# Performance work log

Measured on AMD Instinct MI355X. Metric: run time of the kernel, lower is better.

## Reference

```python
import jax, jax.numpy as jnp
import numpy as np

# Routing structure from the torch module
GT0 = [[0,1,0,0,1,0],[0,1,0,0,0,1],[0,0,1,0,1,0],[0,0,1,0,0,1],[0,0,0,1,1,0],[0,0,0,1,0,1]]
NCLS = 6
K = 1  # top-k

def _expert_pairs():
    # For class i, expert index m = 1+(j-1)*5+(k-1) maps to atom1[j-1] -> atom2[k-1].
    pairs = []
    for i in range(NCLS):
        p = [(j - 1, k - 1) for j in range(1, 6) for k in range(1, 6)
             if j != k and GT0[i][j] == 1 and GT0[i][k] == 1]
        pairs.append(p)
    return pairs

PAIRS = _expert_pairs()  # each class has exactly 2 (atom1, atom2) pairs

B, P, D, H = 64, 256, 768, 3072

def setup_inputs() -> dict:
    key = jax.random.key(0)
    ks = jax.random.split(key, 8)
    s = 0.02
    x = jax.random.normal(ks[0], (B, NCLS + P, D), dtype=jnp.float32)
    mids = jax.random.randint(ks[1], (B,), 0, 6)
    moe0_W1 = jax.random.normal(ks[2], (D, H), dtype=jnp.float32) * s
    moe0_b1 = jnp.zeros((H,), jnp.float32)
    moe0_W2 = jax.random.normal(ks[3], (H, D), dtype=jnp.float32) * s
    moe0_b2 = jnp.zeros((D,), jnp.float32)
    A1_W = jax.random.normal(ks[4], (5, D, H), dtype=jnp.float32) * s  # atom1 linears
    A1_b = jnp.zeros((5, H), jnp.float32)
    A2_W = jax.random.normal(ks[5], (5, H, D), dtype=jnp.float32) * s  # atom2 linears
    A2_b = jnp.zeros((5, D), jnp.float32)
    G_W = jax.random.normal(ks[6], (NCLS, D, 2), dtype=jnp.float32) * s  # per-class gates (2 experts each, no bias)
    return {"x": x, "moe0_W1": moe0_W1, "moe0_b1": moe0_b1, "moe0_W2": moe0_W2,
            "moe0_b2": moe0_b2, "A1_W": A1_W, "A1_b": A1_b, "A2_W": A2_W,
            "A2_b": A2_b, "G_W": G_W, "mids": mids}

def _gelu(t):
    return jax.nn.gelu(t, approximate=False)  # torch nn.GELU default = erf

def reference(x, moe0_W1, moe0_b1, moe0_W2, moe0_b2, A1_W, A1_b, A2_W, A2_b, G_W, mids):
    cls_tokens = x[:, :NCLS]          # [B, 6, D]
    patch_tokens = x[:, NCLS:]        # [B, P, D]
    patch_out = _gelu(patch_tokens @ moe0_W1 + moe0_b1) @ moe0_W2 + moe0_b2  # [B, P, D]
    cls_outs = []
    for i in range(NCLS):
        tok = cls_tokens[:, i]        # [B, D]
        eouts = [ _gelu(tok @ A1_W[a] + A1_b[a]) @ A2_W[c] + A2_b[c] for (a, c) in PAIRS[i] ]
        out = jnp.stack(eouts, axis=-1)                 # [B, D, E=2]
        gate = jax.nn.softmax(tok @ G_W[i], axis=-1)    # [B, E]
        # top-k masking (k=1 < E=2): keep gates strictly above the (k+1)-th largest
        thr = jnp.sort(gate, axis=-1)[..., -(K + 1)]    # [B]
        mask = (gate > thr[..., None]).astype(gate.dtype)
        g = gate * mask
        g = g / jnp.clip(jnp.sum(g, axis=-1, keepdims=True), 1e-6)
        cls_outs.append(jnp.sum(out * g[:, None, :], axis=-1))  # [B, D]
    cls_out = jnp.stack(cls_outs, axis=1)               # [B, 6, D]
    return jnp.concatenate([cls_out, patch_out], axis=1)  # [B, 6+P, D]
```

## Files before the change

kernel.cpp:

```cpp
#include <hip/hip_runtime.h>
#include <hip/hip_bf16.h>

#define DD 768
#define HH 3072
#define BB 64
#define TT 262

typedef __bf16 bf16x8 __attribute__((ext_vector_type(8)));
typedef float f32x4 __attribute__((ext_vector_type(4)));
typedef unsigned short u16;
typedef unsigned int u32;

__device__ __constant__ int A_FIRST[12]  = {0,3, 0,4, 1,3, 1,4, 2,3, 2,4};
__device__ __constant__ int A_SECOND[12] = {3,0, 4,0, 3,1, 4,1, 3,2, 4,2};

__device__ __forceinline__ float gelu_f(float x) {
  float n2t = x * fmaf(x * x, -0.0713548163f, -1.5957691216f);
  return x * __builtin_amdgcn_rcpf(1.0f + __expf(n2t));
}

__device__ __forceinline__ u16 f2bf(float x) {
  u32 u = __builtin_bit_cast(u32, x);
  return (u16)((u + 0x7fffu + ((u >> 16) & 1u)) >> 16);
}

__device__ __forceinline__ void load_lds16(const void* g, void* l) {
  __builtin_amdgcn_global_load_lds(
      (const __attribute__((address_space(1))) void*)g,
      (__attribute__((address_space(3))) void*)l,
      16, 0, 0);
}

#define VMCNT(n) asm volatile("s_waitcnt vmcnt(" #n ")")
#define BAR() __builtin_amdgcn_s_barrier()
#define WAIT_FRAGS() do { asm volatile("s_waitcnt lgkmcnt(0)"); __builtin_amdgcn_sched_barrier(0); } while (0)

template <int IMM>
__device__ __forceinline__ bf16x8 dsr(u32 addr) {
  f32x4 o;
  asm volatile("ds_read_b128 %0, %1 offset:%c2" : "=v"(o) : "v"(addr), "i"(IMM));
  return __builtin_bit_cast(bf16x8, o);
}

__global__ __launch_bounds__(256)
void preproc(const float* __restrict__ x,
             const float* __restrict__ W1, const float* __restrict__ A1W,
             const float* __restrict__ W2, const float* __restrict__ A2W,
             const float* __restrict__ GW,
             __hip_bfloat16* __restrict__ xb,
             __hip_bfloat16* __restrict__ W1t, __hip_bfloat16* __restrict__ A1t,
             __hip_bfloat16* __restrict__ W2t, __hip_bfloat16* __restrict__ A2t,
             int* __restrict__ sel) {
  __shared__ __hip_bfloat16 tile[32][33];
  const int bx = blockIdx.x;
  const int tid = threadIdx.x;
  if (bx < 12576) {
    int i = bx * 256 + tid;
    float4 v = ((const float4*)x)[i];
    union { u16 s[4]; uint2 d; } pk;
    pk.s[0] = f2bf(v.x); pk.s[1] = f2bf(v.y); pk.s[2] = f2bf(v.z); pk.s[3] = f2bf(v.w);
    *(uint2*)((u16*)xb + (size_t)i * 4) = pk.d;
  } else if (bx < 40224) {
    int R, C;
    const float* ip;
    __hip_bfloat16* op;
    int t;
    if (bx < 26400) {
      t = bx - 12576; R = DD; C = HH;
      int z = t / 2304; t %= 2304;
      ip = z ? (A1W + (size_t)(z - 1) * DD * HH) : W1;
      op = z ? (A1t + (size_t)(z - 1) * DD * HH) : W1t;
    } else {
      t = bx - 26400; R = HH; C = DD;
      int z = t / 2304; t %= 2304;
      ip = z ? (A2W + (size_t)(z - 1) * DD * HH) : W2;
      op = z ? (A2t + (size_t)(z - 1) * DD * HH) : W2t;
    }
    int ctiles = C >> 5;
    int c0 = (t % ctiles) * 32, r0 = (t / ctiles) * 32;
    int tx = tid & 31, ty = tid >> 5;
#pragma unroll
    for (int s = 0; s < 4; ++s) {
      int rr = ty * 4 + s;
      tile[rr][tx] = __float2bfloat16(ip[(size_t)(r0 + rr) * C + c0 + tx]);
    }
    __syncthreads();
#pragma unroll
    for (int s = 0; s < 4; ++s) {
      int cc = ty * 4 + s;
      op[(size_t)(c0 + cc) * R + r0 + tx] = tile[tx][cc];
    }
  } else {
    int unit = (bx - 40224) * 4 + (tid >> 6);
    int lane = tid & 63;
    int b = unit & 63, i = unit >> 6;
    const float* tok = x + (size_t)(b * TT + i) * DD;
    const float* g = GW + (size_t)i * DD * 2;
    float p0 = 0.f, p1 = 0.f;
    for (int k = lane; k < DD; k += 64) {
      float tv = tok[k];
      p0 += tv * g[k * 2 + 0];
      p1 += tv * g[k * 2 + 1];
    }
#pragma unroll
    for (int o = 32; o; o >>= 1) { p0 += __shfl_xor(p0, o); p1 += __shfl_xor(p1, o); }
    if (lane == 0) sel[i * 64 + b] = (p0 > p1) ? 0 : ((p1 > p0) ? 1 : 2);
  }
}

template <int R>
__device__ __forceinline__ void rdA4(bf16x8 (&af)[4], u32 a) {
  af[0] = dsr<R + 0>(a);    af[1] = dsr<R + 2048>(a);
  af[2] = dsr<R + 4096>(a); af[3] = dsr<R + 6144>(a);
}
template <int R>
__device__ __forceinline__ void rdB4(bf16x8 (&bf)[4], u32 b) {
  bf[0] = dsr<R + 0>(b);     bf[1] = dsr<R + 2048>(b);
  bf[2] = dsr<R + 16384>(b); bf[3] = dsr<R + 18432>(b);
}

__device__ __forceinline__ void st2r(const char* g, size_t r64, char* smem, int region, int ldsb) {
  load_lds16(g,       smem + region + ldsb);
  load_lds16(g + r64, smem + region + 8192 + ldsb);
}

template <int MH>
__device__ __forceinline__ void mma16(f32x4 (&acc)[8][4], const bf16x8 (&af)[4], const bf16x8 (&bf)[4]) {
  __builtin_amdgcn_s_setprio(1);
#pragma unroll
  for (int ii = 0; ii < 4; ++ii)
#pragma unroll
    for (int j = 0; j < 4; ++j)
      acc[MH * 4 + ii][j] =
          __builtin_amdgcn_mfma_f32_16x16x32_bf16(bf[j], af[ii], acc[MH * 4 + ii][j], 0, 0, 0);
  __builtin_amdgcn_s_setprio(0);
}

template <int MODE>
__device__ __forceinline__
void gemm_big(char* __restrict__ smem, int bx,
              const __hip_bfloat16* __restrict__ A, const __hip_bfloat16* __restrict__ Bw,
              const float* __restrict__ bias, void* __restrict__ Out) {
  constexpr int KDIM = (MODE == 0) ? DD : HH;
  constexpr int KT = KDIM / 64;
  constexpr int ITER = KT / 2;
  constexpr size_t KB = (size_t)KDIM * 2;
  constexpr size_t R64 = 64 * KB, R128 = 128 * KB;
  constexpr int A0S0 = 0, A1S0 = 16384, A0S1 = 32768, A1S1 = 49152;
  constexpr int BB0S0 = 65536, BB1S0 = 81920, BB0S1 = 98304, BB1S1 = 114688;

  const int tid = threadIdx.x;
  const int lane = tid & 63;
  const int q = lane >> 4, r = lane & 15;
  const int wave = tid >> 6;
  const int wave_m = wave >> 2, wave_n = wave & 3;

  int m0, n0;
  if constexpr (MODE == 0) {
    int chunk = bx / 192, local = bx % 192;
    m0 = (chunk * 16 + local % 16) * 256;
    n0 = (local / 16) * 256;
  } else {
    m0 = (bx % 64) * 256;
    n0 = (bx / 64) * 256;
  }

  const int trow = tid >> 3;
  const int sw = ((tid & 7) ^ (trow & 7)) << 4;
  size_t a_row;
  if constexpr (MODE == 0) a_row = (size_t)((m0 >> 8) * TT + 6 + trow);
  else                     a_row = (size_t)(m0 + trow);
  const char* gA = (const char*)A + a_row * KB + sw;
  const char* gB = (const char*)Bw + (size_t)(n0 + trow) * KB + sw;
  const int ldsb = (tid & ~63) * 16;

  const u32 lds0 = (u32)(uintptr_t)smem;
  const u32 aA0 = lds0 + (wave_m * 64 + r) * 128 + ((q ^ (r & 7)) << 4);
  const u32 aA1 = aA0 ^ 64;
  const u32 aB0 = lds0 + 65536 + (wave_n * 32 + r) * 128 + ((q ^ (r & 7)) << 4);
  const u32 aB1 = aB0 ^ 64;

  f32x4 acc[8][4];
#pragma unroll
  for (int i = 0; i < 8; ++i)
#pragma unroll
    for (int j = 0; j < 4; ++j) acc[i][j] = (f32x4){0.f, 0.f, 0.f, 0.f};
  bf16x8 af[4], bf0[4], bf1[4];

  st2r(gA,        R64, smem, A0S0,  ldsb);
  st2r(gB,        R64, smem, BB0S0, ldsb);
  st2r(gB + R128, R64, smem, BB1S0, ldsb);
  st2r(gA + R128, R64, smem, A1S0,  ldsb);
  st2r(gA + 128,  R64, smem, A0S1,  ldsb);
  st2r(gB + 128,  R64, smem, BB0S1, ldsb);
  VMCNT(6);
  BAR();

#pragma unroll 1
  for (int i = 0; i < ITER - 1; ++i) {
    rdA4<A0S0>(af, aA0);
    rdB4<0>(bf0, aB0);
    st2r(gB + R128 + 128, R64, smem, BB1S1, ldsb);
    BAR(); WAIT_FRAGS(); mma16<0>(acc, af, bf0); BAR();
    rdA4<A0S0>(af, aA1);
    rdB4<0>(bf1, aB1);
    st2r(gA + R128 + 128, R64, smem, A1S1, ldsb);
    BAR(); WAIT_FRAGS(); mma16<0>(acc, af, bf1); VMCNT(8); BAR();
    rdA4<A1S0>(af, aA0);
    st2r(gA + 256, R64, smem, A0S0, ldsb);
    BAR(); WAIT_FRAGS(); mma16<1>(acc, af, bf0); BAR();
    rdA4<A1S0>(af, aA1);
    st2r(gB + 256, R64, smem, BB0S0, ldsb);
    BAR(); WAIT_FRAGS(); mma16<1>(acc, af, bf1); VMCNT(6); BAR();
    rdA4<A0S1>(af, aA0);
    rdB4<32768>(bf0, aB0);
    st2r(gB + R128 + 256, R64, smem, BB1S0, ldsb);
    BAR(); WAIT_FRAGS(); mma16<0>(acc, af, bf0); BAR();
    rdA4<A0S1>(af, aA1);
    rdB4<32768>(bf1, aB1);
    st2r(gA + R128 + 256, R64, smem, A1S0, ldsb);
    BAR(); WAIT_FRAGS(); mma16<0>(acc, af, bf1); VMCNT(8); BAR();
    rdA4<A1S1>(af, aA0);
    st2r(gA + 384, R64, smem, A0S1, ldsb);
    BAR(); WAIT_FRAGS(); mma16<1>(acc, af, bf0); BAR();
    rdA4<A1S1>(af, aA1);
    st2r(gB + 384, R64, smem, BB0S1, ldsb);
    BAR(); WAIT_FRAGS(); mma16<1>(acc, af, bf1); VMCNT(6); BAR();
    gA += 256; gB += 256;
  }

  rdA4<A0S0>(af, aA0);
  rdB4<0>(bf0, aB0);
  st2r(gB + R128 + 128, R64, smem, BB1S1, ldsb);
  BAR(); WAIT_FRAGS(); mma16<0>(acc, af, bf0); BAR();
  rdA4<A0S0>(af, aA1);
  rdB4<0>(bf1, aB1);
  st2r(gA + R128 + 128, R64, smem, A1S1, ldsb);
  BAR(); WAIT_FRAGS(); mma16<0>(acc, af, bf1); VMCNT(8); BAR();
  rdA4<A1S0>(af, aA0);
  BAR(); WAIT_FRAGS(); mma16<1>(acc, af, bf0); BAR();
  rdA4<A1S0>(af, aA1);
  BAR(); WAIT_FRAGS(); mma16<1>(acc, af, bf1); VMCNT(2); BAR();
  rdA4<A0S1>(af, aA0);
  rdB4<32768>(bf0, aB0);
  BAR(); WAIT_FRAGS(); mma16<0>(acc, af, bf0); BAR();
  rdA4<A0S1>(af, aA1);
  rdB4<32768>(bf1, aB1);
  BAR(); WAIT_FRAGS(); mma16<0>(acc, af, bf1); VMCNT(0); BAR();
  rdA4<A1S1>(af, aA0);
  BAR(); WAIT_FRAGS(); mma16<1>(acc, af, bf0); BAR();
  rdA4<A1S1>(af, aA1);
  BAR(); WAIT_FRAGS(); mma16<1>(acc, af, bf1);

#pragma unroll
  for (int i = 0; i < 8; ++i) {
    const int m_g = m0 + (i >> 2) * 128 + wave_m * 64 + (i & 3) * 16 + r;
#pragma unroll
    for (int j = 0; j < 4; ++j) {
      const int n_g = n0 + (j >> 1) * 128 + wave_n * 32 + (j & 1) * 16 + q * 4;
      f32x4 v = acc[i][j];
      v += *(const f32x4*)(bias + n_g);
      if constexpr (MODE == 0) {
        union { u16 s[4]; uint2 d; } pk;
#pragma unroll
        for (int rg = 0; rg < 4; ++rg) pk.s[rg] = f2bf(gelu_f(v[rg]));
        *(uint2*)((u16*)Out + (size_t)m_g * HH + n_g) = pk.d;
      } else {
        const int b = m_g >> 8, p = m_g & 255;
        *(f32x4*)((float*)Out + (size_t)(b * TT + 6 + p) * DD + n_g) = v;
      }
    }
  }
}

template <int MODE>
__device__ __forceinline__
void gemm_cls(char* __restrict__ smem, int bx,
              const __hip_bfloat16* __restrict__ A, const __hip_bfloat16* __restrict__ Bw,
              const float* __restrict__ bias, void* __restrict__ Out, const int* __restrict__ sel) {
  constexpr int KDIM = (MODE == 2) ? DD : HH;
  constexpr int KT = KDIM / 64;
  char* As = smem;
  char* Bs = smem + 8192;

  const int tid = threadIdx.x;
  const int lane = tid & 63;
  const int q = lane >> 4, r = lane & 15;
  const int wave = tid >> 6;
  const int wave_m = wave >> 2, wave_n = wave & 3;

  int n0, combo, e;
  if constexpr (MODE == 2) { n0 = (bx % 24) * 128; combo = bx / 24; e = A_FIRST[combo]; }
  else                     { n0 = (bx % 6) * 128;  combo = bx / 6;  e = A_SECOND[combo]; }
  const int cls_i = combo >> 1;
  const __hip_bfloat16* Bp = Bw + (size_t)e * DD * HH;
  const float* biasp = bias + e * ((MODE == 2) ? HH : DD);

  const int trow = tid >> 3;
  const int sw = ((tid & 7) ^ (trow & 7)) << 4;
  const char* gA = (const char*)A +
      ((MODE == 2) ? (size_t)(trow * TT + cls_i) * (DD * 2)
                   : (size_t)(combo * 64 + trow) * (HH * 2)) + sw;
  const char* gB = (const char*)Bp + (size_t)(n0 + trow) * (KDIM * 2) + sw;
  const int ldsb = (tid & ~63) * 16;
  const int sa = (q ^ (r & 7)) << 4;

  f32x4 acc[2][2];
  acc[0][0] = acc[0][1] = acc[1][0] = acc[1][1] = (f32x4){0.f, 0.f, 0.f, 0.f};

  for (int t = 0; t < KT; ++t) {
    load_lds16(gA + t * 128, As + ldsb);
    load_lds16(gB + t * 128, Bs + ldsb);
    load_lds16(gB + (size_t)64 * (KDIM * 2) + t * 128, Bs + 8192 + ldsb);
    __syncthreads();
#pragma unroll
    for (int ks = 0; ks < 2; ++ks) {
      bf16x8 a0 = *(const bf16x8*)(As + (wave_m * 32 + r) * 128 + (sa ^ (ks << 6)));
      bf16x8 a1 = *(const bf16x8*)(As + (wave_m * 32 + 16 + r) * 128 + (sa ^ (ks << 6)));
      bf16x8 b0 = *(const bf16x8*)(Bs + (wave_n * 32 + r) * 128 + (sa ^ (ks << 6)));
      bf16x8 b1 = *(const bf16x8*)(Bs + (wave_n * 32 + 16 + r) * 128 + (sa ^ (ks << 6)));
      acc[0][0] = __builtin_amdgcn_mfma_f32_16x16x32_bf16(b0, a0, acc[0][0], 0, 0, 0);
      acc[0][1] = __builtin_amdgcn_mfma_f32_16x16x32_bf16(b1, a0, acc[0][1], 0, 0, 0);
      acc[1][0] = __builtin_amdgcn_mfma_f32_16x16x32_bf16(b0, a1, acc[1][0], 0, 0, 0);
      acc[1][1] = __builtin_amdgcn_mfma_f32_16x16x32_bf16(b1, a1, acc[1][1], 0, 0, 0);
    }
    __syncthreads();
  }

#pragma unroll
  for (int i = 0; i < 2; ++i) {
    const int m_g = wave_m * 32 + i * 16 + r;
#pragma unroll
    for (int j = 0; j < 2; ++j) {
      const int n_g = n0 + wave_n * 32 + j * 16 + q * 4;
      f32x4 v = acc[i][j];
      v += *(const f32x4*)(biasp + n_g);
      if constexpr (MODE == 2) {
        union { u16 s[4]; uint2 d; } pk;
#pragma unroll
        for (int rg = 0; rg < 4; ++rg) pk.s[rg] = f2bf(gelu_f(v[rg]));
        *(uint2*)((u16*)Out + (size_t)(combo * 64 + m_g) * HH + n_g) = pk.d;
      } else {
        const int s = sel[cls_i * 64 + m_g];
        const int jj = combo & 1;
        float* dst = (float*)Out + (size_t)(m_g * TT + cls_i) * DD + n_g;
        if (s == jj)                    *(f32x4*)dst = v;
        else if (jj == 0 && s == 2)     *(f32x4*)dst = (f32x4){0.f, 0.f, 0.f, 0.f};
      }
    }
  }
}

__global__ __launch_bounds__(512, 2)
void mega1(const __hip_bfloat16* __restrict__ xb, const __hip_bfloat16* __restrict__ W1t,
           const float* __restrict__ b1, __hip_bfloat16* __restrict__ hid,
           const __hip_bfloat16* __restrict__ A1t, const float* __restrict__ A1b,
           __hip_bfloat16* __restrict__ hcls) {
  __shared__ __align__(16) char smem[131072];
  int bx = blockIdx.x;
  if (bx < 768) gemm_big<0>(smem, bx, xb, W1t, b1, hid);
  else          gemm_cls<2>(smem, bx - 768, xb, A1t, A1b, hcls, nullptr);
}

__global__ __launch_bounds__(512, 2)
void mega2(const __hip_bfloat16* __restrict__ hid, const __hip_bfloat16* __restrict__ W2t,
           const float* __restrict__ b2, float* __restrict__ out,
           const __hip_bfloat16* __restrict__ hcls, const __hip_bfloat16* __restrict__ A2t,
           const float* __restrict__ A2b, const int* __restrict__ sel) {
  __shared__ __align__(16) char smem[131072];
  int bx = blockIdx.x;
  if (bx < 192) gemm_big<1>(smem, bx, hid, W2t, b2, out);
  else          gemm_cls<3>(smem, bx - 192, hcls, A2t, A2b, out, sel);
}

extern "C" void kernel_launch(void* const* d_in, const int* in_sizes, int n_in,
                              void* d_out, int out_size, void* d_ws, size_t ws_size,
                              hipStream_t stream) {
  const float* x   = (const float*)d_in[0];
  const float* W1  = (const float*)d_in[1];
  const float* b1  = (const float*)d_in[2];
  const float* W2  = (const float*)d_in[3];
  const float* b2  = (const float*)d_in[4];
  const float* A1W = (const float*)d_in[5];
  const float* A1b = (const float*)d_in[6];
  const float* A2W = (const float*)d_in[7];
  const float* A2b = (const float*)d_in[8];
  const float* GW  = (const float*)d_in[9];
  float* out = (float*)d_out;

  char* ws = (char*)d_ws;
  __hip_bfloat16* xb   = (__hip_bfloat16*)(ws + 0);
  __hip_bfloat16* W1t  = (__hip_bfloat16*)(ws + 25755648);
  __hip_bfloat16* W2t  = (__hip_bfloat16*)(ws + 30474240);
  __hip_bfloat16* A1t  = (__hip_bfloat16*)(ws + 35192832);
  __hip_bfloat16* A2t  = (__hip_bfloat16*)(ws + 58785792);
  __hip_bfloat16* hcls = (__hip_bfloat16*)(ws + 82378752);
  int* sel             = (int*)(ws + 87097344);
  __hip_bfloat16* hid  = (__hip_bfloat16*)(ws + 87099136);

  preproc<<<40320, 256, 0, stream>>>(x, W1, A1W, W2, A2W, GW, xb, W1t, A1t, W2t, A2t, sel);
  mega1<<<1056, 512, 0, stream>>>(xb, W1t, b1, hid, A1t, A1b, hcls);
  mega2<<<264, 512, 0, stream>>>(hid, W2t, b2, out, hcls, A2t, A2b, sel);
}
```

Measured before the change: 387.2 us.

## Replace first-stage GEMMs with generic smaller-tile single-buffered GEMM body

Adds a templated gemm_body that mega1 now uses for both the patch up-projection (128x256 tiles, 256 threads) and the class-token A1 projections (64x128 tiles). It replaces the double-buffered, priority-scheduled 256x256 kernel and the separate cls kernel. The aim is smaller tiles, more blocks and lower LDS use so more blocks fit per CU. The cost is losing the software pipelining, since each k-step now has a load, a barrier, compute and another barrier. The old gemm_big and gemm_cls templates are trimmed down to the second-stage modes only.

```diff
diff --git a/kernel.cpp b/kernel.cpp
--- a/kernel.cpp
+++ b/kernel.cpp
@@ -108,6 +108,122 @@
   }
 }
 
+template <int BM, int BN, int MODE>
+__device__ __forceinline__
+void gemm_body(char* __restrict__ smem, int bx,
+               const __hip_bfloat16* __restrict__ A,
+               const __hip_bfloat16* __restrict__ Bw,
+               const float* __restrict__ bias,
+               void* __restrict__ Out,
+               const int* __restrict__ sel) {
+  constexpr int KDIM = DD;
+  constexpr int KITERS = KDIM / 64;
+  constexpr int WAVES_M = (BM == 128) ? 2 : 1;
+  constexpr int WAVES_N = 4 / WAVES_M;
+  constexpr int MT = BM / (16 * WAVES_M);
+  constexpr int NT = BN / (16 * WAVES_N);
+  constexpr int CHA = BM / 32;
+  constexpr int CHB = BN / 32;
+
+  char* As = smem;
+  char* Bs = smem + BM * 128;
+
+  const int tid = threadIdx.x;
+  const int lane = tid & 63;
+  const int wave = tid >> 6;
+  const int q = lane >> 4;
+  const int r = lane & 15;
+  const int wave_m = wave / WAVES_N;
+  const int wave_n = wave % WAVES_N;
+
+  int m0 = 0, n0, combo = 0, cls_i = 0;
+  const __hip_bfloat16* Bp = Bw;
+  const float* biasp = bias;
+  if constexpr (MODE == 0) {
+    int chunk = bx / 192, local = bx % 192;
+    int nb = local / 16, mloc = local % 16;
+    m0 = (chunk * 16 + mloc) * BM;
+    n0 = nb * BN;
+  } else {
+    n0 = (bx % 24) * BN;
+    combo = bx / 24;
+    cls_i = combo >> 1;
+    int e = A_FIRST[combo];
+    Bp = Bw + (size_t)e * DD * HH;
+    biasp = bias + e * HH;
+  }
+
+  const int trow = tid >> 3;
+  const int sw = ((tid & 7) ^ (trow & 7)) << 4;
+  size_t a_row_off;
+  if constexpr (MODE == 0) {
+    int m = m0 + trow;
+    a_row_off = (size_t)((m >> 8) * TT + 6 + (m & 255)) * DD * 2;
+  } else {
+    a_row_off = (size_t)(trow * TT + cls_i) * DD * 2;
+  }
+  const char* gA0 = (const char*)A + a_row_off + sw;
+  const char* gB0 = (const char*)Bp + (size_t)(n0 + trow) * KDIM * 2 + sw;
+  constexpr size_t ASTR = (size_t)32 * ((MODE == 0) ? DD : TT * DD) * 2;
+  constexpr size_t BSTR = (size_t)32 * KDIM * 2;
+  const int wave_base = (tid & ~63) * 16;
+
+  f32x4 acc[MT][NT];
+#pragma unroll
+  for (int i_ = 0; i_ < MT; ++i_)
+#pragma unroll
+    for (int j_ = 0; j_ < NT; ++j_) acc[i_][j_] = (f32x4){0.f, 0.f, 0.f, 0.f};
+
+  const char* a_rd = As + (wave_m * (MT * 16) + r) * 128;
+  const char* b_rd = Bs + (wave_n * (NT * 16) + r) * 128;
+  const int sa = ((q ^ (r & 7)) << 4);
+
+  for (int kt = 0; kt < KITERS; ++kt) {
+#pragma unroll
+    for (int u = 0; u < CHA; ++u) load_lds16(gA0 + u * ASTR, As + u * 4096 + wave_base);
+#pragma unroll
+    for (int u = 0; u < CHB; ++u) load_lds16(gB0 + u * BSTR, Bs + u * 4096 + wave_base);
+    gA0 += 128;
+    gB0 += 128;
+    __syncthreads();
+#pragma unroll
+    for (int t = 0; t < 2; ++t) {
+      const int so = sa ^ (t << 6);
+      bf16x8 af[MT], bf[NT];
+#pragma unroll
+      for (int i_ = 0; i_ < MT; ++i_) af[i_] = *(const bf16x8*)(a_rd + i_ * 2048 + so);
+#pragma unroll
+      for (int j_ = 0; j_ < NT; ++j_) bf[j_] = *(const bf16x8*)(b_rd + j_ * 2048 + so);
+#pragma unroll
+      for (int i_ = 0; i_ < MT; ++i_)
+#pragma unroll
+        for (int j_ = 0; j_ < NT; ++j_)
+          acc[i_][j_] = __builtin_amdgcn_mfma_f32_16x16x32_bf16(bf[j_], af[i_], acc[i_][j_], 0, 0, 0);
+    }
+    __syncthreads();
+  }
+
+#pragma unroll
+  for (int i_ = 0; i_ < MT; ++i_) {
+    int m_g = m0 + wave_m * (MT * 16) + i_ * 16 + r;
+#pragma unroll
+    for (int j_ = 0; j_ < NT; ++j_) {
+      int nb = n0 + wave_n * (NT * 16) + j_ * 16 + q * 4;
+      f32x4 v = acc[i_][j_];
+      f32x4 bb = *(const f32x4*)(biasp + nb);
+      v += bb;
+      union { u16 s[4]; uint2 d; } pk;
+#pragma unroll
+      for (int rg = 0; rg < 4; ++rg) pk.s[rg] = f2bf(gelu_f(v[rg]));
+      if constexpr (MODE == 0) {
+        *(uint2*)((u16*)Out + (size_t)m_g * HH + nb) = pk.d;
+      } else {
+        *(uint2*)((u16*)Out + (size_t)(combo * 64 + m_g) * HH + nb) = pk.d;
+      }
+    }
+  }
+}
+
 template <int R>
 __device__ __forceinline__ void rdA4(bf16x8 (&af)[4], u32 a) {
   af[0] = dsr<R + 0>(a);    af[1] = dsr<R + 2048>(a);
@@ -141,7 +257,7 @@
 void gemm_big(char* __restrict__ smem, int bx,
               const __hip_bfloat16* __restrict__ A, const __hip_bfloat16* __restrict__ Bw,
               const float* __restrict__ bias, void* __restrict__ Out) {
-  constexpr int KDIM = (MODE == 0) ? DD : HH;
+  constexpr int KDIM = HH;
   constexpr int KT = KDIM / 64;
   constexpr int ITER = KT / 2;
   constexpr size_t KB = (size_t)KDIM * 2;
@@ -155,22 +271,12 @@
   const int wave = tid >> 6;
   const int wave_m = wave >> 2, wave_n = wave & 3;
 
-  int m0, n0;
-  if constexpr (MODE == 0) {
-    int chunk = bx / 192, local = bx % 192;
-    m0 = (chunk * 16 + local % 16) * 256;
-    n0 = (local / 16) * 256;
-  } else {
-    m0 = (bx % 64) * 256;
-    n0 = (bx / 64) * 256;
-  }
+  const int m0 = (bx % 64) * 256;
+  const int n0 = (bx / 64) * 256;
 
   const int trow = tid >> 3;
   const int sw = ((tid & 7) ^ (trow & 7)) << 4;
-  size_t a_row;
-  if constexpr (MODE == 0) a_row = (size_t)((m0 >> 8) * TT + 6 + trow);
-  else                     a_row = (size_t)(m0 + trow);
-  const char* gA = (const char*)A + a_row * KB + sw;
+  const char* gA = (const char*)A + (size_t)(m0 + trow) * KB + sw;
   const char* gB = (const char*)Bw + (size_t)(n0 + trow) * KB + sw;
   const int ldsb = (tid & ~63) * 16;
 
@@ -260,15 +366,8 @@
       const int n_g = n0 + (j >> 1) * 128 + wave_n * 32 + (j & 1) * 16 + q * 4;
       f32x4 v = acc[i][j];
       v += *(const f32x4*)(bias + n_g);
-      if constexpr (MODE == 0) {
-        union { u16 s[4]; uint2 d; } pk;
-#pragma unroll
-        for (int rg = 0; rg < 4; ++rg) pk.s[rg] = f2bf(gelu_f(v[rg]));
-        *(uint2*)((u16*)Out + (size_t)m_g * HH + n_g) = pk.d;
-      } else {
-        const int b = m_g >> 8, p = m_g & 255;
-        *(f32x4*)((float*)Out + (size_t)(b * TT + 6 + p) * DD + n_g) = v;
-      }
+      const int b = m_g >> 8, p = m_g & 255;
+      *(f32x4*)((float*)Out + (size_t)(b * TT + 6 + p) * DD + n_g) = v;
     }
   }
 }
@@ -278,7 +377,7 @@
 void gemm_cls(char* __restrict__ smem, int bx,
               const __hip_bfloat16* __restrict__ A, const __hip_bfloat16* __restrict__ Bw,
               const float* __restrict__ bias, void* __restrict__ Out, const int* __restrict__ sel) {
-  constexpr int KDIM = (MODE == 2) ? DD : HH;
+  constexpr int KDIM = HH;
   constexpr int KT = KDIM / 64;
   char* As = smem;
   char* Bs = smem + 8192;
@@ -289,18 +388,16 @@
   const int wave = tid >> 6;
   const int wave_m = wave >> 2, wave_n = wave & 3;
 
-  int n0, combo, e;
-  if constexpr (MODE == 2) { n0 = (bx % 24) * 128; combo = bx / 24; e = A_FIRST[combo]; }
-  else                     { n0 = (bx % 6) * 128;  combo = bx / 6;  e = A_SECOND[combo]; }
+  const int n0 = (bx % 6) * 128;
+  const int combo = bx / 6;
+  const int e = A_SECOND[combo];
   const int cls_i = combo >> 1;
   const __hip_bfloat16* Bp = Bw + (size_t)e * DD * HH;
-  const float* biasp = bias + e * ((MODE == 2) ? HH : DD);
+  const float* biasp = bias + e * DD;
 
   const int trow = tid >> 3;
   const int sw = ((tid & 7) ^ (trow & 7)) << 4;
-  const char* gA = (const char*)A +
-      ((MODE == 2) ? (size_t)(trow * TT + cls_i) * (DD * 2)
-                   : (size_t)(combo * 64 + trow) * (HH * 2)) + sw;
+  const char* gA = (const char*)A + (size_t)(combo * 64 + trow) * (HH * 2) + sw;
   const char* gB = (const char*)Bp + (size_t)(n0 + trow) * (KDIM * 2) + sw;
   const int ldsb = (tid & ~63) * 16;
   const int sa = (q ^ (r & 7)) << 4;
@@ -335,31 +432,24 @@
       const int n_g = n0 + wave_n * 32 + j * 16 + q * 4;
       f32x4 v = acc[i][j];
       v += *(const f32x4*)(biasp + n_g);
-      if constexpr (MODE == 2) {
-        union { u16 s[4]; uint2 d; } pk;
-#pragma unroll
-        for (int rg = 0; rg < 4; ++rg) pk.s[rg] = f2bf(gelu_f(v[rg]));
-        *(uint2*)((u16*)Out + (size_t)(combo * 64 + m_g) * HH + n_g) = pk.d;
-      } else {
-        const int s = sel[cls_i * 64 + m_g];
-        const int jj = combo & 1;
-        float* dst = (float*)Out + (size_t)(m_g * TT + cls_i) * DD + n_g;
-        if (s == jj)                    *(f32x4*)dst = v;
-        else if (jj == 0 && s == 2)     *(f32x4*)dst = (f32x4){0.f, 0.f, 0.f, 0.f};
-      }
-    }
-  }
-}
-
-__global__ __launch_bounds__(512, 2)
+      const int s = sel[cls_i * 64 + m_g];
+      const int jj = combo & 1;
+      float* dst = (float*)Out + (size_t)(m_g * TT + cls_i) * DD + n_g;
+      if (s == jj)                    *(f32x4*)dst = v;
+      else if (jj == 0 && s == 2)     *(f32x4*)dst = (f32x4){0.f, 0.f, 0.f, 0.f};
+    }
+  }
+}
+
+__global__ __launch_bounds__(256, 2)
 void mega1(const __hip_bfloat16* __restrict__ xb, const __hip_bfloat16* __restrict__ W1t,
            const float* __restrict__ b1, __hip_bfloat16* __restrict__ hid,
            const __hip_bfloat16* __restrict__ A1t, const float* __restrict__ A1b,
            __hip_bfloat16* __restrict__ hcls) {
-  __shared__ __align__(16) char smem[131072];
+  __shared__ __align__(16) char smem[(128 + 256) * 128];
   int bx = blockIdx.x;
-  if (bx < 768) gemm_big<0>(smem, bx, xb, W1t, b1, hid);
-  else          gemm_cls<2>(smem, bx - 768, xb, A1t, A1b, hcls, nullptr);
+  if (bx < 1536) gemm_body<128, 256, 0>(smem, bx, xb, W1t, b1, hid, nullptr);
+  else           gemm_body<64, 128, 2>(smem, bx - 1536, xb, A1t, A1b, hcls, nullptr);
 }
 
 __global__ __launch_bounds__(512, 2)
@@ -399,6 +489,6 @@
   __hip_bfloat16* hid  = (__hip_bfloat16*)(ws + 87099136);
 
   preproc<<<40320, 256, 0, stream>>>(x, W1, A1W, W2, A2W, GW, xb, W1t, A1t, W2t, A2t, sel);
-  mega1<<<1056, 512, 0, stream>>>(xb, W1t, b1, hid, A1t, A1b, hcls);
+  mega1<<<1824, 256, 0, stream>>>(xb, W1t, b1, hid, A1t, A1b, hcls);
   mega2<<<264, 512, 0, stream>>>(hid, W2t, b2, out, hcls, A2t, A2b, sel);
 }
```

Measured after the change: 387.8 us. Within noise of the previous version (+0.1%).
